# Kernel tuning notes

Hardware: AMD Instinct MI355X
Metric: run time of the kernel (lower is better)

Reference implementation:

```python
import jax, jax.numpy as jnp
import numpy as np

B = 128        # batch (images/texts)
N = 2048       # other texts per image
F_IMG = 1024   # raw image feature dim (abstracted encoder input)
F_TXT = 512    # raw text feature dim
D = 512        # embedding dim (num_features=512 in BasicNet)
TOPK = B - 1   # default topK = batch - 1


def setup_inputs() -> dict:
    key = jax.random.key(0)
    ks = jax.random.split(key, 6)
    return {
        "input_images": jax.random.normal(ks[0], (B, F_IMG), jnp.float32),
        "input_texts": jax.random.normal(ks[1], (B, F_TXT), jnp.float32),
        "other_texts": jax.random.normal(ks[2], (B, N, F_TXT), jnp.float32),
        "W_img": jax.random.normal(ks[3], (F_IMG, D), jnp.float32) / np.float32(np.sqrt(F_IMG)),
        "W_txt": jax.random.normal(ks[4], (F_TXT, D), jnp.float32) / np.float32(np.sqrt(F_TXT)),
        "logit_scale": jnp.asarray(np.log(1.0 / 0.07), jnp.float32),
    }


def reference(input_images, input_texts, other_texts, W_img, W_txt, logit_scale):
    K = TOPK
    # encoders abstracted as linear projections to D=512
    img = input_images @ W_img                                   # [B, D]
    img = img / jnp.linalg.norm(img, axis=1, keepdims=True)      # L2-normalize images
    txt = input_texts @ W_txt                                    # [B, D]
    txt = txt / jnp.linalg.norm(txt, axis=1, keepdims=True)      # row-wise norm == norm after concat
    oth = jnp.einsum('bnf,fd->bnd', other_texts, W_txt)          # [B, N, D]
    oth = oth / jnp.linalg.norm(oth, axis=2, keepdims=True)

    scale = jnp.exp(logit_scale)
    logit_in = scale * jnp.sum(img * txt, axis=1)                # [B] image_i . text_i
    logit_oth = scale * jnp.einsum('bd,bnd->bn', img, oth)       # [B, N]

    # descending sort + take top-K (lax.top_k returns sorted descending)
    topk_vals, _ = jax.lax.top_k(logit_oth, K)                   # [B, K]

    # indices = sorted(range(K) + [min(i, K-1)]): duplicate element p=min(i,K-1)
    rows = jnp.arange(B)
    cols = jnp.arange(K + 1)[None, :]                            # [1, K+1]
    p = jnp.minimum(rows, K - 1)[:, None]                        # [B, 1]
    gidx = jnp.where(cols <= p, cols, cols - 1)                  # [B, K+1]
    gathered = jnp.take_along_axis(topk_vals, gidx, axis=1)      # [B, K+1]

    # overwrite column i of row i with the positive (input text) logit
    out = jnp.where(cols == rows[:, None], logit_in[:, None], gathered)
    return out
```

## Files before the change

kernel.cpp:

```cpp
#include <hip/hip_runtime.h>
#include <hip/hip_bf16.h>
#include <math.h>

#define B_SZ 128
#define N_OTH 2048
#define F_IMG 1024
#define F_TXT 512
#define D_EMB 512

typedef __attribute__((ext_vector_type(8))) short short8;
typedef __attribute__((ext_vector_type(16))) float f32x16;

static __device__ __forceinline__ ushort f2bf(float f) {
    __hip_bfloat16 h = __float2bfloat16(f);
    return *reinterpret_cast<ushort*>(&h);
}

__global__ __launch_bounds__(512) void k_prep(const float* __restrict__ in_img,
                                              const float* __restrict__ in_txt,
                                              const float* __restrict__ W_img,
                                              const float* __restrict__ W_txt,
                                              const float* __restrict__ p_ls,
                                              float* __restrict__ img,
                                              float* __restrict__ logit_in,
                                              ushort* __restrict__ wf) {
    if (blockIdx.x >= B_SZ) {
        const int g = (blockIdx.x - B_SZ) * 512 + threadIdx.x;
        const int l = g & 63;
        const int frag = g >> 6;
        const int kstep = frag >> 4;
        const int ct = frag & 15;
        const int col = ct * 32 + (l & 31);
        const int kb = kstep * 16 + (l >> 5) * 8;
        short8 o;
#pragma unroll
        for (int j = 0; j < 8; ++j) o[j] = (short)f2bf(W_txt[(kb + j) * D_EMB + col]);
        *(short8*)(wf + (size_t)g * 8) = o;
        return;
    }
    const int b = blockIdx.x;
    const int d = threadIdx.x;
    __shared__ float row[F_IMG];
    __shared__ float wsum[8];
    __shared__ float s_rn;
    const int lane = d & 63, wv = d >> 6;

    for (int i = d; i < F_IMG; i += 512) row[i] = in_img[b * F_IMG + i];
    __syncthreads();
    float acc = 0.f;
#pragma unroll 8
    for (int f = 0; f < F_IMG; ++f) acc = fmaf(row[f], W_img[f * D_EMB + d], acc);
    float sq = acc * acc;
#pragma unroll
    for (int off = 32; off > 0; off >>= 1) sq += __shfl_down(sq, off);
    if (lane == 0) wsum[wv] = sq;
    __syncthreads();
    if (d == 0) {
        float s = 0.f;
        for (int w = 0; w < 8; ++w) s += wsum[w];
        s_rn = 1.0f / sqrtf(s);
    }
    __syncthreads();
    const float iv = acc * s_rn;
    img[b * D_EMB + d] = iv;

    __syncthreads();
    row[d] = in_txt[b * F_TXT + d];
    __syncthreads();
    float tacc = 0.f;
#pragma unroll 8
    for (int f = 0; f < F_TXT; ++f) tacc = fmaf(row[f], W_txt[f * D_EMB + d], tacc);
    float tsq = tacc * tacc;
#pragma unroll
    for (int off = 32; off > 0; off >>= 1) tsq += __shfl_down(tsq, off);
    __syncthreads();
    if (lane == 0) wsum[wv] = tsq;
    __syncthreads();
    if (d == 0) {
        float s = 0.f;
        for (int w = 0; w < 8; ++w) s += wsum[w];
        s_rn = 1.0f / sqrtf(s);
    }
    __syncthreads();
    float pd = (tacc * s_rn) * iv;
#pragma unroll
    for (int off = 32; off > 0; off >>= 1) pd += __shfl_down(pd, off);
    __syncthreads();
    if (lane == 0) wsum[wv] = pd;
    __syncthreads();
    if (d == 0) {
        float s = 0.f;
        for (int w = 0; w < 8; ++w) s += wsum[w];
        logit_in[b] = expf(p_ls[0]) * s;
    }
}

__device__ __forceinline__ void loadA(const float* gs, float4 v[4]) {
    v[0] = *(const float4*)(gs + 0);
    v[1] = *(const float4*)(gs + 4);
    v[2] = *(const float4*)(gs + 8);
    v[3] = *(const float4*)(gs + 12);
}
__device__ __forceinline__ void cvtWrite(char* buf, int wb0, int wb1, const float4 v[4]) {
    short8 p0, p1;
    p0[0] = (short)f2bf(v[0].x); p0[1] = (short)f2bf(v[0].y); p0[2] = (short)f2bf(v[0].z); p0[3] = (short)f2bf(v[0].w);
    p0[4] = (short)f2bf(v[1].x); p0[5] = (short)f2bf(v[1].y); p0[6] = (short)f2bf(v[1].z); p0[7] = (short)f2bf(v[1].w);
    p1[0] = (short)f2bf(v[2].x); p1[1] = (short)f2bf(v[2].y); p1[2] = (short)f2bf(v[2].z); p1[3] = (short)f2bf(v[2].w);
    p1[4] = (short)f2bf(v[3].x); p1[5] = (short)f2bf(v[3].y); p1[6] = (short)f2bf(v[3].z); p1[7] = (short)f2bf(v[3].w);
    *(short8*)(buf + wb0) = p0;
    *(short8*)(buf + wb1) = p1;
}

__global__ __launch_bounds__(512, 2) void k_gemm(const float* __restrict__ oth,
                                                 const ushort* __restrict__ wf,
                                                 const float* __restrict__ img,
                                                 float* __restrict__ numA,
                                                 float* __restrict__ denA) {
    __shared__ ushort sA[2][128 * 64];
    __shared__ float redN[8][128];
    __shared__ float redD[8][128];
    const int tid = threadIdx.x;
    const int l = tid & 63;
    const int wv = tid >> 6;
    const int b = blockIdx.x >> 4;
    const size_t row0 = (size_t)blockIdx.x * 128;

    const int srow = tid >> 2;
    const int sk0 = (tid & 3) * 16;
    const float* gsrc = oth + (row0 + srow) * F_TXT + sk0;
    const int swz = (srow & 7) << 4;
    const int wb0 = srow * 128 + ((sk0 * 2 + 0) ^ swz);
    const int wb1 = srow * 128 + ((sk0 * 2 + 16) ^ swz);

    int rowbase[4];
#pragma unroll
    for (int m = 0; m < 4; ++m) rowbase[m] = (m * 32 + (l & 31)) * 128;
    int koff[4];
#pragma unroll
    for (int ks = 0; ks < 4; ++ks) koff[ks] = ((ks * 32 + (l >> 5) * 16) ^ ((l & 7) << 4));

    f32x16 acc[4][2];
#pragma unroll
    for (int m = 0; m < 4; ++m)
#pragma unroll
        for (int n = 0; n < 2; ++n)
#pragma unroll
            for (int r = 0; r < 16; ++r) acc[m][n][r] = 0.f;

    float4 va[4];
    short8 bfr[4][2];

    loadA(gsrc, va);
#pragma unroll
    for (int ks = 0; ks < 4; ++ks)
#pragma unroll
        for (int n = 0; n < 2; ++n)
            bfr[ks][n] = *(const short8*)(wf + ((size_t)(ks * 16 + wv * 2 + n) * 64 + l) * 8);
    cvtWrite((char*)sA[0], wb0, wb1, va);
    __syncthreads();

#pragma unroll
    for (int t = 0; t < 8; ++t) {
        const int cur = t & 1;
        if (t < 7) loadA(gsrc + (t + 1) * 64, va);
        __builtin_amdgcn_sched_barrier(0);
        __builtin_amdgcn_s_setprio(1);
#pragma unroll
        for (int ks = 0; ks < 4; ++ks) {
            short8 af[4];
#pragma unroll
            for (int m = 0; m < 4; ++m)
                af[m] = *(const short8*)((const char*)sA[cur] + rowbase[m] + koff[ks]);
#pragma unroll
            for (int m = 0; m < 4; ++m)
#pragma unroll
                for (int n = 0; n < 2; ++n)
                    acc[m][n] = __builtin_amdgcn_mfma_f32_32x32x16_bf16(af[m], bfr[ks][n], acc[m][n], 0, 0, 0);
        }
        __builtin_amdgcn_s_setprio(0);
        __builtin_amdgcn_sched_barrier(0);
        if (t < 7) {
#pragma unroll
            for (int ks = 0; ks < 4; ++ks)
#pragma unroll
                for (int n = 0; n < 2; ++n)
                    bfr[ks][n] = *(const short8*)(wf + ((size_t)((t + 1) * 64 + ks * 16 + wv * 2 + n) * 64 + l) * 8);
            __builtin_amdgcn_sched_barrier(0);
            cvtWrite((char*)sA[cur ^ 1], wb0, wb1, va);
            asm volatile("s_waitcnt lgkmcnt(0)" ::: "memory");
            __builtin_amdgcn_sched_barrier(0);
            __builtin_amdgcn_s_barrier();
            __builtin_amdgcn_sched_barrier(0);
        }
    }

    const float ic0 = img[b * D_EMB + wv * 64 + (l & 31)];
    const float ic1 = img[b * D_EMB + wv * 64 + 32 + (l & 31)];
#pragma unroll
    for (int m = 0; m < 4; ++m) {
#pragma unroll
        for (int rg = 0; rg < 16; ++rg) {
            const float p = acc[m][0][rg];
            const float q = acc[m][1][rg];
            float tn = p * ic0 + q * ic1;
            float td = p * p + q * q;
#pragma unroll
            for (int off = 1; off <= 16; off <<= 1) {
                tn += __shfl_xor(tn, off);
                td += __shfl_xor(td, off);
            }
            if ((l & 31) == 0) {
                const int r = m * 32 + (rg & 3) + 8 * (rg >> 2) + 4 * (l >> 5);
                redN[wv][r] = tn;
                redD[wv][r] = td;
            }
        }
    }
    __syncthreads();
    if (tid < 128) {
        float tn = 0.f, td = 0.f;
#pragma unroll
        for (int w = 0; w < 8; ++w) { tn += redN[w][tid]; td += redD[w][tid]; }
        numA[row0 + tid] = tn;
        denA[row0 + tid] = td;
    }
}

__global__ __launch_bounds__(512) void k_topk(const float* __restrict__ numA,
                                              const float* __restrict__ denA,
                                              const float* __restrict__ logit_in,
                                              const float* __restrict__ p_ls,
                                              float* __restrict__ out) {
    const int b = blockIdx.x;
    const int tid = threadIdx.x;
    const float scale = expf(p_ls[0]);
    __shared__ float a[N_OTH];
    for (int i = tid; i < N_OTH; i += 512) {
        const float nu = numA[(size_t)b * N_OTH + i];
        const float de = denA[(size_t)b * N_OTH + i];
        a[i] = scale * nu / sqrtf(de);
    }
    __syncthreads();
    for (unsigned k = 2; k <= N_OTH; k <<= 1) {
        for (unsigned j = k >> 1; j > 0; j >>= 1) {
#pragma unroll
            for (int s = 0; s < N_OTH / 512; ++s) {
                const unsigned i = tid + s * 512u;
                const unsigned ixj = i ^ j;
                if (ixj > i) {
                    const bool asc = ((i & k) == 0);
                    const float x = a[i], y = a[ixj];
                    if ((x > y) == asc) { a[i] = y; a[ixj] = x; }
                }
            }
            __syncthreads();
        }
    }
    if (tid < 128) {
        const int j = tid;
        float v;
        if (j == b) {
            v = logit_in[b];
        } else {
            const int m = j - (j > b ? 1 : 0);
            v = a[N_OTH - 1 - m];
        }
        out[b * 128 + j] = v;
    }
}

extern "C" void kernel_launch(void* const* d_in, const int* in_sizes, int n_in,
                              void* d_out, int out_size, void* d_ws, size_t ws_size,
                              hipStream_t stream) {
    const float* in_img = (const float*)d_in[0];
    const float* in_txt = (const float*)d_in[1];
    const float* oth    = (const float*)d_in[2];
    const float* W_img  = (const float*)d_in[3];
    const float* W_txt  = (const float*)d_in[4];
    const float* p_ls   = (const float*)d_in[5];
    float* out = (float*)d_out;

    float* ws = (float*)d_ws;
    float* img      = ws;
    float* logit_in = ws + 65536;
    float* numA     = ws + 65536 + 128;
    float* denA     = numA + 262144;
    ushort* wfrag   = (ushort*)(denA + 262144);

    k_prep<<<B_SZ + 64, 512, 0, stream>>>(in_img, in_txt, W_img, W_txt, p_ls, img, logit_in, wfrag);
    k_gemm<<<(B_SZ * N_OTH) / 128, 512, 0, stream>>>(oth, wfrag, img, numA, denA);
    k_topk<<<B_SZ, 512, 0, stream>>>(numA, denA, logit_in, p_ls, out);
}
```

Measured before the change: 399.9 us.

## Restructure GEMM with direct-to-LDS fp32 loads, triple buffering, and D-split blocks

The projection GEMM now copies fp32 other_texts straight into LDS with global_load_lds into a triple-buffered swizzled tile. The bf16 conversion moves to the point where A fragments are read from LDS. Each 64-row strip is split across two blocks that each cover half of the embedding dimension, writing partial numerator and denominator sums that the top-k kernel adds. The aim is to take staging through registers off the critical path and raise occupancy. The cost is that each pair of blocks reads the same A strip twice, and the split adds extra partial-sum traffic.

Measured after the change: 391.3 us. 2.1% less time.

```diff
diff --git a/kernel.cpp b/kernel.cpp
--- a/kernel.cpp
+++ b/kernel.cpp
@@ -7,6 +7,7 @@
 #define F_IMG 1024
 #define F_TXT 512
 #define D_EMB 512
+#define TOT (B_SZ * N_OTH)
 
 typedef __attribute__((ext_vector_type(8))) short short8;
 typedef __attribute__((ext_vector_type(16))) float f32x16;
@@ -14,6 +15,11 @@
 static __device__ __forceinline__ ushort f2bf(float f) {
     __hip_bfloat16 h = __float2bfloat16(f);
     return *reinterpret_cast<ushort*>(&h);
+}
+
+static __device__ __forceinline__ void glds16(const float* g, float* l) {
+    __builtin_amdgcn_global_load_lds((const __attribute__((address_space(1))) void*)g,
+                                     (__attribute__((address_space(3))) void*)l, 16, 0, 0);
 }
 
 __global__ __launch_bounds__(512) void k_prep(const float* __restrict__ in_img,
@@ -95,98 +101,91 @@
     }
 }
 
-__device__ __forceinline__ void loadA(const float* gs, float4 v[4]) {
-    v[0] = *(const float4*)(gs + 0);
-    v[1] = *(const float4*)(gs + 4);
-    v[2] = *(const float4*)(gs + 8);
-    v[3] = *(const float4*)(gs + 12);
-}
-__device__ __forceinline__ void cvtWrite(char* buf, int wb0, int wb1, const float4 v[4]) {
-    short8 p0, p1;
-    p0[0] = (short)f2bf(v[0].x); p0[1] = (short)f2bf(v[0].y); p0[2] = (short)f2bf(v[0].z); p0[3] = (short)f2bf(v[0].w);
-    p0[4] = (short)f2bf(v[1].x); p0[5] = (short)f2bf(v[1].y); p0[6] = (short)f2bf(v[1].z); p0[7] = (short)f2bf(v[1].w);
-    p1[0] = (short)f2bf(v[2].x); p1[1] = (short)f2bf(v[2].y); p1[2] = (short)f2bf(v[2].z); p1[3] = (short)f2bf(v[2].w);
-    p1[4] = (short)f2bf(v[3].x); p1[5] = (short)f2bf(v[3].y); p1[6] = (short)f2bf(v[3].z); p1[7] = (short)f2bf(v[3].w);
-    *(short8*)(buf + wb0) = p0;
-    *(short8*)(buf + wb1) = p1;
-}
-
-__global__ __launch_bounds__(512, 2) void k_gemm(const float* __restrict__ oth,
+__global__ __launch_bounds__(256, 3) void k_gemm(const float* __restrict__ oth,
                                                  const ushort* __restrict__ wf,
                                                  const float* __restrict__ img,
                                                  float* __restrict__ numA,
                                                  float* __restrict__ denA) {
-    __shared__ ushort sA[2][128 * 64];
-    __shared__ float redN[8][128];
-    __shared__ float redD[8][128];
+    __shared__ float sA[3][64 * 64];
+    __shared__ float redN[4][64];
+    __shared__ float redD[4][64];
     const int tid = threadIdx.x;
     const int l = tid & 63;
     const int wv = tid >> 6;
-    const int b = blockIdx.x >> 4;
-    const size_t row0 = (size_t)blockIdx.x * 128;
-
-    const int srow = tid >> 2;
-    const int sk0 = (tid & 3) * 16;
-    const float* gsrc = oth + (row0 + srow) * F_TXT + sk0;
-    const int swz = (srow & 7) << 4;
-    const int wb0 = srow * 128 + ((sk0 * 2 + 0) ^ swz);
-    const int wb1 = srow * 128 + ((sk0 * 2 + 16) ^ swz);
-
-    int rowbase[4];
-#pragma unroll
-    for (int m = 0; m < 4; ++m) rowbase[m] = (m * 32 + (l & 31)) * 128;
-    int koff[4];
-#pragma unroll
-    for (int ks = 0; ks < 4; ++ks) koff[ks] = ((ks * 32 + (l >> 5) * 16) ^ ((l & 7) << 4));
-
-    f32x16 acc[4][2];
-#pragma unroll
-    for (int m = 0; m < 4; ++m)
+    const int strip = blockIdx.x >> 1;
+    const int h = blockIdx.x & 1;
+    const int b = strip >> 5;
+    const size_t row0 = (size_t)strip * 64;
+
+    const float* gA[4];
+#pragma unroll
+    for (int j = 0; j < 4; ++j) {
+        const int row = wv * 16 + j * 4 + (l >> 4);
+        const int gcol = (l & 15) ^ (row & 7);
+        gA[j] = oth + (row0 + row) * F_TXT + gcol * 4;
+    }
+
+    const ushort* wbase = wf + ((size_t)(h * 8 + wv * 2) * 64 + l) * 8;
+
+    f32x16 acc[2][2];
+#pragma unroll
+    for (int m = 0; m < 2; ++m)
 #pragma unroll
         for (int n = 0; n < 2; ++n)
 #pragma unroll
             for (int r = 0; r < 16; ++r) acc[m][n][r] = 0.f;
 
-    float4 va[4];
-    short8 bfr[4][2];
-
-    loadA(gsrc, va);
-#pragma unroll
-    for (int ks = 0; ks < 4; ++ks)
-#pragma unroll
-        for (int n = 0; n < 2; ++n)
-            bfr[ks][n] = *(const short8*)(wf + ((size_t)(ks * 16 + wv * 2 + n) * 64 + l) * 8);
-    cvtWrite((char*)sA[0], wb0, wb1, va);
-    __syncthreads();
+#pragma unroll
+    for (int j = 0; j < 4; ++j) glds16(gA[j] + 0 * 64, &sA[0][(wv * 16 + j * 4) * 64]);
+#pragma unroll
+    for (int j = 0; j < 4; ++j) glds16(gA[j] + 1 * 64, &sA[1][(wv * 16 + j * 4) * 64]);
+    __builtin_amdgcn_sched_barrier(0);
+    asm volatile("s_waitcnt vmcnt(4)" ::: "memory");
+    __builtin_amdgcn_sched_barrier(0);
+    __builtin_amdgcn_s_barrier();
+    __builtin_amdgcn_sched_barrier(0);
 
 #pragma unroll
     for (int t = 0; t < 8; ++t) {
-        const int cur = t & 1;
-        if (t < 7) loadA(gsrc + (t + 1) * 64, va);
+        const int cur = t % 3;
+        short8 bfr[4][2];
+#pragma unroll
+        for (int ks = 0; ks < 4; ++ks)
+#pragma unroll
+            for (int n = 0; n < 2; ++n)
+                bfr[ks][n] = *(const short8*)(wbase + (size_t)((t * 4 + ks) * 16 + n) * 512);
+        __builtin_amdgcn_sched_barrier(0);
+        if (t < 6) {
+#pragma unroll
+            for (int j = 0; j < 4; ++j)
+                glds16(gA[j] + (t + 2) * 64, &sA[(t + 2) % 3][(wv * 16 + j * 4) * 64]);
+        }
         __builtin_amdgcn_sched_barrier(0);
         __builtin_amdgcn_s_setprio(1);
 #pragma unroll
         for (int ks = 0; ks < 4; ++ks) {
-            short8 af[4];
-#pragma unroll
-            for (int m = 0; m < 4; ++m)
-                af[m] = *(const short8*)((const char*)sA[cur] + rowbase[m] + koff[ks]);
-#pragma unroll
-            for (int m = 0; m < 4; ++m)
+            short8 af[2];
+#pragma unroll
+            for (int m = 0; m < 2; ++m) {
+                const int r = m * 32 + (l & 31);
+                const int g0 = ks * 4 + (l >> 5) * 2;
+                const float4 fa = *(const float4*)&sA[cur][r * 64 + ((g0 ^ (r & 7)) << 2)];
+                const float4 fb = *(const float4*)&sA[cur][r * 64 + (((g0 + 1) ^ (r & 7)) << 2)];
+                short8 v;
+                v[0] = (short)f2bf(fa.x); v[1] = (short)f2bf(fa.y);
+                v[2] = (short)f2bf(fa.z); v[3] = (short)f2bf(fa.w);
+                v[4] = (short)f2bf(fb.x); v[5] = (short)f2bf(fb.y);
+                v[6] = (short)f2bf(fb.z); v[7] = (short)f2bf(fb.w);
+                af[m] = v;
+            }
+#pragma unroll
+            for (int m = 0; m < 2; ++m)
 #pragma unroll
                 for (int n = 0; n < 2; ++n)
                     acc[m][n] = __builtin_amdgcn_mfma_f32_32x32x16_bf16(af[m], bfr[ks][n], acc[m][n], 0, 0, 0);
         }
         __builtin_amdgcn_s_setprio(0);
-        __builtin_amdgcn_sched_barrier(0);
         if (t < 7) {
-#pragma unroll
-            for (int ks = 0; ks < 4; ++ks)
-#pragma unroll
-                for (int n = 0; n < 2; ++n)
-                    bfr[ks][n] = *(const short8*)(wf + ((size_t)((t + 1) * 64 + ks * 16 + wv * 2 + n) * 64 + l) * 8);
-            __builtin_amdgcn_sched_barrier(0);
-            cvtWrite((char*)sA[cur ^ 1], wb0, wb1, va);
             asm volatile("s_waitcnt lgkmcnt(0)" ::: "memory");
             __builtin_amdgcn_sched_barrier(0);
             __builtin_amdgcn_s_barrier();
@@ -194,15 +193,17 @@
         }
     }
 
-    const float ic0 = img[b * D_EMB + wv * 64 + (l & 31)];
-    const float ic1 = img[b * D_EMB + wv * 64 + 32 + (l & 31)];
-#pragma unroll
-    for (int m = 0; m < 4; ++m) {
+    float ic[2];
+#pragma unroll
+    for (int n = 0; n < 2; ++n)
+        ic[n] = img[b * D_EMB + h * 256 + wv * 64 + n * 32 + (l & 31)];
+#pragma unroll
+    for (int m = 0; m < 2; ++m) {
 #pragma unroll
         for (int rg = 0; rg < 16; ++rg) {
             const float p = acc[m][0][rg];
             const float q = acc[m][1][rg];
-            float tn = p * ic0 + q * ic1;
+            float tn = p * ic[0] + q * ic[1];
             float td = p * p + q * q;
 #pragma unroll
             for (int off = 1; off <= 16; off <<= 1) {
@@ -217,12 +218,12 @@
         }
     }
     __syncthreads();
-    if (tid < 128) {
+    if (tid < 64) {
         float tn = 0.f, td = 0.f;
 #pragma unroll
-        for (int w = 0; w < 8; ++w) { tn += redN[w][tid]; td += redD[w][tid]; }
-        numA[row0 + tid] = tn;
-        denA[row0 + tid] = td;
+        for (int w = 0; w < 4; ++w) { tn += redN[w][tid]; td += redD[w][tid]; }
+        numA[(size_t)h * TOT + row0 + tid] = tn;
+        denA[(size_t)h * TOT + row0 + tid] = td;
     }
 }
 
@@ -236,8 +237,9 @@
     const float scale = expf(p_ls[0]);
     __shared__ float a[N_OTH];
     for (int i = tid; i < N_OTH; i += 512) {
-        const float nu = numA[(size_t)b * N_OTH + i];
-        const float de = denA[(size_t)b * N_OTH + i];
+        const size_t idx = (size_t)b * N_OTH + i;
+        const float nu = numA[idx] + numA[TOT + idx];
+        const float de = denA[idx] + denA[TOT + idx];
         a[i] = scale * nu / sqrtf(de);
     }
     __syncthreads();
@@ -284,10 +286,10 @@
     float* img      = ws;
     float* logit_in = ws + 65536;
     float* numA     = ws + 65536 + 128;
-    float* denA     = numA + 262144;
-    ushort* wfrag   = (ushort*)(denA + 262144);
+    float* denA     = numA + 2 * TOT;
+    ushort* wfrag   = (ushort*)(denA + 2 * TOT);
 
     k_prep<<<B_SZ + 64, 512, 0, stream>>>(in_img, in_txt, W_img, W_txt, p_ls, img, logit_in, wfrag);
-    k_gemm<<<(B_SZ * N_OTH) / 128, 512, 0, stream>>>(oth, wfrag, img, numA, denA);
+    k_gemm<<<(TOT / 64) * 2, 256, 0, stream>>>(oth, wfrag, img, numA, denA);
     k_topk<<<B_SZ, 512, 0, stream>>>(numA, denA, logit_in, p_ls, out);
 }
```

## Split GEMM over output-column quarters with 16x16 MFMA and atomic reduction

Applied to the files above, without the earlier changes.

The GEMM kernel moves from 128-row tiles covering all 512 output columns to 64-row tiles where each of four blocks handles 128 columns. It switches from 32x32x16 to 16x16x32 bf16 MFMA, uses 256-thread blocks, and merges partial numerator/denominator sums with atomicAdd after a memset. The aim is more blocks and better occupancy. In exchange, each A row is loaded and converted to bf16 four times instead of once, and atomics plus a memset are added.

Measured after the change: 414.0 us. +3.5%, slower.

```diff
diff --git a/kernel.cpp b/kernel.cpp
--- a/kernel.cpp
+++ b/kernel.cpp
@@ -7,9 +7,10 @@
 #define F_IMG 1024
 #define F_TXT 512
 #define D_EMB 512
+#define TOT (B_SZ * N_OTH)
 
 typedef __attribute__((ext_vector_type(8))) short short8;
-typedef __attribute__((ext_vector_type(16))) float f32x16;
+typedef __attribute__((ext_vector_type(4))) float f32x4;
 
 static __device__ __forceinline__ ushort f2bf(float f) {
     __hip_bfloat16 h = __float2bfloat16(f);
@@ -28,10 +29,10 @@
         const int g = (blockIdx.x - B_SZ) * 512 + threadIdx.x;
         const int l = g & 63;
         const int frag = g >> 6;
-        const int kstep = frag >> 4;
-        const int ct = frag & 15;
-        const int col = ct * 32 + (l & 31);
-        const int kb = kstep * 16 + (l >> 5) * 8;
+        const int kk = frag >> 5;
+        const int ct = frag & 31;
+        const int col = ct * 16 + (l & 15);
+        const int kb = kk * 32 + (l >> 4) * 8;
         short8 o;
 #pragma unroll
         for (int j = 0; j < 8; ++j) o[j] = (short)f2bf(W_txt[(kb + j) * D_EMB + col]);
@@ -111,19 +112,21 @@
     *(short8*)(buf + wb1) = p1;
 }
 
-__global__ __launch_bounds__(512, 2) void k_gemm(const float* __restrict__ oth,
+__global__ __launch_bounds__(256, 4) void k_gemm(const float* __restrict__ oth,
                                                  const ushort* __restrict__ wf,
                                                  const float* __restrict__ img,
                                                  float* __restrict__ numA,
                                                  float* __restrict__ denA) {
-    __shared__ ushort sA[2][128 * 64];
-    __shared__ float redN[8][128];
-    __shared__ float redD[8][128];
+    __shared__ ushort sA[2][64 * 64];
+    __shared__ float redN[4][64];
+    __shared__ float redD[4][64];
     const int tid = threadIdx.x;
     const int l = tid & 63;
     const int wv = tid >> 6;
-    const int b = blockIdx.x >> 4;
-    const size_t row0 = (size_t)blockIdx.x * 128;
+    const int strip = blockIdx.x >> 2;
+    const int h = blockIdx.x & 3;
+    const int b = strip >> 5;
+    const size_t row0 = (size_t)strip * 64;
 
     const int srow = tid >> 2;
     const int sk0 = (tid & 3) * 16;
@@ -132,30 +135,32 @@
     const int wb0 = srow * 128 + ((sk0 * 2 + 0) ^ swz);
     const int wb1 = srow * 128 + ((sk0 * 2 + 16) ^ swz);
 
+    const ushort* wbase = wf + ((size_t)(h * 8 + wv * 2) * 64 + l) * 8;
+
     int rowbase[4];
 #pragma unroll
-    for (int m = 0; m < 4; ++m) rowbase[m] = (m * 32 + (l & 31)) * 128;
-    int koff[4];
-#pragma unroll
-    for (int ks = 0; ks < 4; ++ks) koff[ks] = ((ks * 32 + (l >> 5) * 16) ^ ((l & 7) << 4));
-
-    f32x16 acc[4][2];
+    for (int m = 0; m < 4; ++m) rowbase[m] = (m * 16 + (l & 15)) * 128;
+    int koff[2];
+#pragma unroll
+    for (int kkl = 0; kkl < 2; ++kkl)
+        koff[kkl] = ((kkl * 64 + (l >> 4) * 16) ^ ((l & 7) << 4));
+
+    f32x4 acc[4][2];
 #pragma unroll
     for (int m = 0; m < 4; ++m)
 #pragma unroll
         for (int n = 0; n < 2; ++n)
-#pragma unroll
-            for (int r = 0; r < 16; ++r) acc[m][n][r] = 0.f;
+            acc[m][n] = (f32x4){0.f, 0.f, 0.f, 0.f};
 
     float4 va[4];
-    short8 bfr[4][2];
+    short8 bfr[2][2];
 
     loadA(gsrc, va);
 #pragma unroll
-    for (int ks = 0; ks < 4; ++ks)
+    for (int kkl = 0; kkl < 2; ++kkl)
 #pragma unroll
         for (int n = 0; n < 2; ++n)
-            bfr[ks][n] = *(const short8*)(wf + ((size_t)(ks * 16 + wv * 2 + n) * 64 + l) * 8);
+            bfr[kkl][n] = *(const short8*)(wbase + (size_t)(kkl * 16384 + n * 512));
     cvtWrite((char*)sA[0], wb0, wb1, va);
     __syncthreads();
 
@@ -164,65 +169,62 @@
         const int cur = t & 1;
         if (t < 7) loadA(gsrc + (t + 1) * 64, va);
         __builtin_amdgcn_sched_barrier(0);
-        __builtin_amdgcn_s_setprio(1);
-#pragma unroll
-        for (int ks = 0; ks < 4; ++ks) {
+#pragma unroll
+        for (int kkl = 0; kkl < 2; ++kkl) {
             short8 af[4];
 #pragma unroll
             for (int m = 0; m < 4; ++m)
-                af[m] = *(const short8*)((const char*)sA[cur] + rowbase[m] + koff[ks]);
+                af[m] = *(const short8*)((const char*)sA[cur] + rowbase[m] + koff[kkl]);
 #pragma unroll
             for (int m = 0; m < 4; ++m)
 #pragma unroll
                 for (int n = 0; n < 2; ++n)
-                    acc[m][n] = __builtin_amdgcn_mfma_f32_32x32x16_bf16(af[m], bfr[ks][n], acc[m][n], 0, 0, 0);
-        }
-        __builtin_amdgcn_s_setprio(0);
+                    acc[m][n] = __builtin_amdgcn_mfma_f32_16x16x32_bf16(af[m], bfr[kkl][n], acc[m][n], 0, 0, 0);
+        }
         __builtin_amdgcn_sched_barrier(0);
         if (t < 7) {
 #pragma unroll
-            for (int ks = 0; ks < 4; ++ks)
+            for (int kkl = 0; kkl < 2; ++kkl)
 #pragma unroll
                 for (int n = 0; n < 2; ++n)
-                    bfr[ks][n] = *(const short8*)(wf + ((size_t)((t + 1) * 64 + ks * 16 + wv * 2 + n) * 64 + l) * 8);
+                    bfr[kkl][n] = *(const short8*)(wbase + (size_t)(((t + 1) * 2 + kkl) * 16384 + n * 512));
             __builtin_amdgcn_sched_barrier(0);
             cvtWrite((char*)sA[cur ^ 1], wb0, wb1, va);
-            asm volatile("s_waitcnt lgkmcnt(0)" ::: "memory");
-            __builtin_amdgcn_sched_barrier(0);
-            __builtin_amdgcn_s_barrier();
-            __builtin_amdgcn_sched_barrier(0);
-        }
-    }
-
-    const float ic0 = img[b * D_EMB + wv * 64 + (l & 31)];
-    const float ic1 = img[b * D_EMB + wv * 64 + 32 + (l & 31)];
+        }
+        __syncthreads();
+    }
+
+    float ic[2];
+#pragma unroll
+    for (int n = 0; n < 2; ++n)
+        ic[n] = img[b * D_EMB + h * 128 + wv * 32 + n * 16 + (l & 15)];
 #pragma unroll
     for (int m = 0; m < 4; ++m) {
 #pragma unroll
-        for (int rg = 0; rg < 16; ++rg) {
-            const float p = acc[m][0][rg];
-            const float q = acc[m][1][rg];
-            float tn = p * ic0 + q * ic1;
-            float td = p * p + q * q;
-#pragma unroll
-            for (int off = 1; off <= 16; off <<= 1) {
+        for (int rg = 0; rg < 4; ++rg) {
+            const float pv = acc[m][0][rg];
+            const float qv = acc[m][1][rg];
+            float tn = pv * ic[0] + qv * ic[1];
+            float td = pv * pv + qv * qv;
+#pragma unroll
+            for (int off = 1; off <= 8; off <<= 1) {
                 tn += __shfl_xor(tn, off);
                 td += __shfl_xor(td, off);
             }
-            if ((l & 31) == 0) {
-                const int r = m * 32 + (rg & 3) + 8 * (rg >> 2) + 4 * (l >> 5);
+            if ((l & 15) == 0) {
+                const int r = m * 16 + (l >> 4) * 4 + rg;
                 redN[wv][r] = tn;
                 redD[wv][r] = td;
             }
         }
     }
     __syncthreads();
-    if (tid < 128) {
+    if (tid < 64) {
         float tn = 0.f, td = 0.f;
 #pragma unroll
-        for (int w = 0; w < 8; ++w) { tn += redN[w][tid]; td += redD[w][tid]; }
-        numA[row0 + tid] = tn;
-        denA[row0 + tid] = td;
+        for (int w = 0; w < 4; ++w) { tn += redN[w][tid]; td += redD[w][tid]; }
+        atomicAdd(&numA[row0 + tid], tn);
+        atomicAdd(&denA[row0 + tid], td);
     }
 }
 
@@ -236,9 +238,8 @@
     const float scale = expf(p_ls[0]);
     __shared__ float a[N_OTH];
     for (int i = tid; i < N_OTH; i += 512) {
-        const float nu = numA[(size_t)b * N_OTH + i];
-        const float de = denA[(size_t)b * N_OTH + i];
-        a[i] = scale * nu / sqrtf(de);
+        const size_t idx = (size_t)b * N_OTH + i;
+        a[i] = scale * numA[idx] / sqrtf(denA[idx]);
     }
     __syncthreads();
     for (unsigned k = 2; k <= N_OTH; k <<= 1) {
@@ -284,10 +285,11 @@
     float* img      = ws;
     float* logit_in = ws + 65536;
     float* numA     = ws + 65536 + 128;
-    float* denA     = numA + 262144;
-    ushort* wfrag   = (ushort*)(denA + 262144);
-
+    float* denA     = numA + TOT;
+    ushort* wfrag   = (ushort*)(denA + TOT);
+
+    hipMemsetAsync(numA, 0, (size_t)2 * TOT * sizeof(float), stream);
     k_prep<<<B_SZ + 64, 512, 0, stream>>>(in_img, in_txt, W_img, W_txt, p_ls, img, logit_in, wfrag);
-    k_gemm<<<(B_SZ * N_OTH) / 128, 512, 0, stream>>>(oth, wfrag, img, numA, denA);
+    k_gemm<<<(TOT / 64) * 4, 256, 0, stream>>>(oth, wfrag, img, numA, denA);
     k_topk<<<B_SZ, 512, 0, stream>>>(numA, denA, logit_in, p_ls, out);
 }
```
